# Optimization experiments

Measured on AMD Instinct MI355X. Metric: run time of the kernel, lower is better.

Reference implementation:

```python
import jax, jax.numpy as jnp
import numpy as np

B, HQ, HKV, D = 32, 32, 8, 128
PAGE_SIZE, PAGES_PER_SEQ = 16, 128
NUM_PAGES = B * PAGES_PER_SEQ
MAX_LEN = PAGE_SIZE * PAGES_PER_SEQ  # 2048
SCALING = 0.08838834764831845  # 1/sqrt(128)
LOGIT_CAP = 50.0


def setup_inputs() -> dict:
    key = jax.random.key(0)
    ks = jax.random.split(key, 6)
    q = jax.random.normal(ks[0], (B, HQ * D), jnp.float32)
    k = jax.random.normal(ks[1], (B, HKV * D), jnp.float32)
    v = jax.random.normal(ks[2], (B, HKV * D), jnp.float32)
    k_cache = jax.random.normal(ks[3], (NUM_PAGES, PAGE_SIZE, HKV, D), jnp.float32)
    v_cache = jax.random.normal(ks[4], (NUM_PAGES, PAGE_SIZE, HKV, D), jnp.float32)
    # disjoint page assignment: request b owns pages [b*128, (b+1)*128)
    page_table = jnp.arange(NUM_PAGES, dtype=jnp.int32).reshape(B, PAGES_PER_SEQ)
    seq_lens = jax.random.randint(ks[5], (B,), 1, MAX_LEN + 1, dtype=jnp.int32)
    return dict(q=q, k=k, v=v, k_cache=k_cache, v_cache=v_cache,
                page_table=page_table, seq_lens=seq_lens)


def reference(q, k, v, k_cache, v_cache, page_table, seq_lens):
    # mirror RadixAttention.forward's k.view(-1, Hkv, D) / v.view(-1, Hkv, D)
    kn = k.reshape(B, HKV, D)
    vn = v.reshape(B, HKV, D)

    # save_kv_cache=True: scatter new token (at position seq_len-1) into paged cache
    pos = seq_lens - 1
    page = page_table[jnp.arange(B), pos // PAGE_SIZE]  # [B]
    slot = pos % PAGE_SIZE                              # [B]
    k_cache = k_cache.at[page, slot].set(kn)
    v_cache = v_cache.at[page, slot].set(vn)

    # gather paged KV per request: [B, Lmax, Hkv, D]
    Kb = k_cache[page_table].reshape(B, MAX_LEN, HKV, D)
    Vb = v_cache[page_table].reshape(B, MAX_LEN, HKV, D)

    # GQA: query head h maps to kv head h // (HQ//HKV)
    G = HQ // HKV
    qh = q.reshape(B, HKV, G, D)
    scores = jnp.einsum('bkgd,blkd->bkgl', qh, Kb) * SCALING  # [B,Hkv,G,L]
    scores = LOGIT_CAP * jnp.tanh(scores / LOGIT_CAP)          # logit capping

    valid = jnp.arange(MAX_LEN, dtype=jnp.int32)[None, :] < seq_lens[:, None]  # [B,L]
    scores = jnp.where(valid[:, None, None, :], scores, -jnp.inf)
    p = jax.nn.softmax(scores, axis=-1)
    out = jnp.einsum('bkgl,blkd->bkgd', p, Vb)  # [B,Hkv,G,D]
    return out.reshape(B, HQ * D)
```

## Files before the change

### kernel.cpp

```cpp
#include <hip/hip_runtime.h>
#include <hip/hip_bf16.h>
#include <math.h>

#define BB 32
#define HQ 32
#define HKV 8
#define DD 128
#define PAGE_SZ 16
#define PAGES_PER_SEQ 128
#define MAX_LEN 2048
#define GG 4
#define NCHUNK 8
#define CHUNK 256
#define SCALING 0.08838834764831845f
#define CAP 50.0f
#define WS_STRIDE 520

__device__ __forceinline__ float dpp8_sum(float x) {
    int t;
    t = __builtin_amdgcn_update_dpp(0, __float_as_int(x), 0x111, 0xF, 0xF, true);
    x += __int_as_float(t);
    t = __builtin_amdgcn_update_dpp(0, __float_as_int(x), 0x112, 0xF, 0xF, true);
    x += __int_as_float(t);
    t = __builtin_amdgcn_update_dpp(0, __float_as_int(x), 0x114, 0xF, 0xF, true);
    x += __int_as_float(t);
    return x;
}

__global__ __launch_bounds__(256, 4) void attn_partial(
    const float* __restrict__ q,
    const float* __restrict__ knew,
    const float* __restrict__ vnew,
    const float* __restrict__ k_cache,
    const float* __restrict__ v_cache,
    const int* __restrict__ page_table,
    const int* __restrict__ seq_lens,
    float* __restrict__ ws)
{
    const int idx = blockIdx.x;
    const int c  = idx % NCHUNK;
    const int bh = idx / NCHUNK;
    const int h  = bh % HKV;
    const int b  = bh / HKV;

    const int L  = seq_lens[b];
    const int t0 = c * CHUNK;
    const int t1 = min(t0 + CHUNK, L);
    float* wsb = ws + (size_t)idx * WS_STRIDE;

    if (t0 >= t1) {
        if (threadIdx.x < GG) { wsb[threadIdx.x] = -INFINITY; wsb[GG + threadIdx.x] = 0.0f; }
        return;
    }
    const int NT = t1 - t0;

    __shared__ float s_q[GG][DD];
    __shared__ float s_sc[GG][CHUNK];
    __shared__ float s_red[8][GG * DD];
    __shared__ int   s_pages[CHUNK / PAGE_SZ];
    __shared__ float s_m[GG], s_l[GG];

    const int tid = threadIdx.x;

    for (int i = tid; i < GG * DD; i += 256) {
        int g = i / DD, d = i % DD;
        s_q[g][d] = q[(size_t)b * (HQ * DD) + (h * GG + g) * DD + d];
    }
    if (tid < CHUNK / PAGE_SZ)
        s_pages[tid] = page_table[b * PAGES_PER_SEQ + t0 / PAGE_SZ + tid];
    __syncthreads();

    const float* knew_row = &knew[(size_t)b * (HKV * DD) + h * DD];
    const float* vnew_row = &vnew[(size_t)b * (HKV * DD) + h * DD];

    {
        const int wv = tid >> 6;
        const int ln = tid & 63;
        const int tg = ln >> 3;
        const int lg = ln & 7;

        float4 qf[GG][4];
        #pragma unroll
        for (int g = 0; g < GG; g++)
            #pragma unroll
            for (int p = 0; p < 4; p++)
                qf[g][p] = *(const float4*)&s_q[g][p * 32 + lg * 4];

        const int niter = (NT + 31) >> 5;

#define LOAD_K(I, KV, WT) do {                                                \
        int t_ = t0 + (I) * 32 + wv * 8 + tg;                                 \
        bool vld_ = t_ < t1;                                                  \
        int tc_ = vld_ ? t_ : (t1 - 1);                                       \
        const float* row_;                                                    \
        if (tc_ == L - 1) row_ = knew_row;                                    \
        else {                                                                \
            int page_ = s_pages[(tc_ - t0) >> 4];                             \
            int slot_ = tc_ & (PAGE_SZ - 1);                                  \
            row_ = &k_cache[((size_t)page_ * PAGE_SZ + slot_) * (HKV * DD) + h * DD]; \
        }                                                                     \
        const float4* r4_ = (const float4*)row_;                              \
        KV[0] = r4_[lg]; KV[1] = r4_[8 + lg];                                 \
        KV[2] = r4_[16 + lg]; KV[3] = r4_[24 + lg];                           \
        WT = vld_ ? (t_ - t0) : -1;                                           \
    } while (0)

        float4 kva[4];
        int wta;
        LOAD_K(0, kva, wta);

        for (int i = 0; i < niter; i++) {
            float4 kvb[4];
            int wtb = -1;
            if (i + 1 < niter) LOAD_K(i + 1, kvb, wtb);

            float dots[GG];
            #pragma unroll
            for (int g = 0; g < GG; g++) {
                float s = 0.0f;
                #pragma unroll
                for (int p = 0; p < 4; p++)
                    s += kva[p].x * qf[g][p].x + kva[p].y * qf[g][p].y
                       + kva[p].z * qf[g][p].z + kva[p].w * qf[g][p].w;
                dots[g] = dpp8_sum(s);
            }
            if (lg == 7 && wta >= 0) {
                #pragma unroll
                for (int g = 0; g < GG; g++) s_sc[g][wta] = dots[g];
            }
            #pragma unroll
            for (int p = 0; p < 4; p++) kva[p] = kvb[p];
            wta = wtb;
        }
#undef LOAD_K
    }
    __syncthreads();

    {
        int g  = tid >> 6;
        int wl = tid & 63;
        float mx = -INFINITY;
        for (int t = wl; t < NT; t += 64) {
            float s = s_sc[g][t];
            s = CAP * tanhf(s * (SCALING * (1.0f / CAP)));
            s_sc[g][t] = s;
            mx = fmaxf(mx, s);
        }
        #pragma unroll
        for (int m = 1; m < 64; m <<= 1) mx = fmaxf(mx, __shfl_xor(mx, m));
        float sum = 0.0f;
        for (int t = wl; t < NT; t += 64) {
            float e = __expf(s_sc[g][t] - mx);
            s_sc[g][t] = e;
            sum += e;
        }
        #pragma unroll
        for (int m = 1; m < 64; m <<= 1) sum += __shfl_xor(sum, m);
        if (wl == 0) { s_m[g] = mx; s_l[g] = sum; }
    }
    __syncthreads();

    const int hw = tid >> 5;
    const int ln = tid & 31;

    float4 acc[GG];
    #pragma unroll
    for (int g = 0; g < GG; g++) acc[g] = make_float4(0.f, 0.f, 0.f, 0.f);

    for (int i = 0; i < CHUNK / 32; i++) {
        const int tbase = t0 + i * 32 + hw;
        if (t0 + i * 32 >= t1) break;

        float4 vv[4];
        int   trel[4];
        bool  vld[4];
        #pragma unroll
        for (int j = 0; j < 4; j++) {
            int t = tbase + j * 8;
            vld[j] = (t < t1);
            int tc = vld[j] ? t : tbase;
            trel[j] = tc - t0;
            const float4* vrow;
            if (tc == L - 1) {
                vrow = (const float4*)vnew_row;
            } else {
                int page = s_pages[trel[j] >> 4];
                int slot = tc & (PAGE_SZ - 1);
                vrow = (const float4*)&v_cache[((size_t)page * PAGE_SZ + slot) * (HKV * DD) + h * DD];
            }
            vv[j] = vrow[ln];
        }
        float p[4][GG];
        #pragma unroll
        for (int j = 0; j < 4; j++)
            #pragma unroll
            for (int g = 0; g < GG; g++)
                p[j][g] = vld[j] ? s_sc[g][trel[j]] : 0.0f;

        #pragma unroll
        for (int j = 0; j < 4; j++) {
            #pragma unroll
            for (int g = 0; g < GG; g++) {
                acc[g].x += p[j][g] * vv[j].x; acc[g].y += p[j][g] * vv[j].y;
                acc[g].z += p[j][g] * vv[j].z; acc[g].w += p[j][g] * vv[j].w;
            }
        }
    }
    #pragma unroll
    for (int g = 0; g < GG; g++)
        *(float4*)&s_red[hw][g * DD + 4 * ln] = acc[g];
    __syncthreads();

    for (int i = tid; i < GG * DD; i += 256) {
        float s = 0.f;
        #pragma unroll
        for (int w = 0; w < 8; w++) s += s_red[w][i];
        wsb[8 + i] = s;
    }
    if (tid < GG) { wsb[tid] = s_m[tid]; wsb[GG + tid] = s_l[tid]; }
}

__global__ __launch_bounds__(512) void attn_combine(
    const float* __restrict__ ws, float* __restrict__ out)
{
    const int bh = blockIdx.x;
    const int h  = bh % HKV;
    const int b  = bh / HKV;
    const int tid = threadIdx.x;
    const int g = tid / DD;
    const int d = tid % DD;

    float mv[NCHUNK], lv[NCHUNK];
    float M = -INFINITY;
    #pragma unroll
    for (int c = 0; c < NCHUNK; c++) {
        const float* wsb = ws + (size_t)(bh * NCHUNK + c) * WS_STRIDE;
        mv[c] = wsb[g];
        lv[c] = wsb[GG + g];
        if (lv[c] > 0.0f) M = fmaxf(M, mv[c]);
    }
    float lsum = 0.0f, osum = 0.0f;
    #pragma unroll
    for (int c = 0; c < NCHUNK; c++) {
        if (lv[c] > 0.0f) {
            const float* wsb = ws + (size_t)(bh * NCHUNK + c) * WS_STRIDE;
            float a = __expf(mv[c] - M);
            lsum += lv[c] * a;
            osum += wsb[8 + g * DD + d] * a;
        }
    }
    out[(size_t)b * (HQ * DD) + (h * GG + g) * DD + d] = osum / lsum;
}

extern "C" void kernel_launch(void* const* d_in, const int* in_sizes, int n_in,
                              void* d_out, int out_size, void* d_ws, size_t ws_size,
                              hipStream_t stream) {
    const float* q       = (const float*)d_in[0];
    const float* k       = (const float*)d_in[1];
    const float* v       = (const float*)d_in[2];
    const float* k_cache = (const float*)d_in[3];
    const float* v_cache = (const float*)d_in[4];
    const int* page_table = (const int*)d_in[5];
    const int* seq_lens   = (const int*)d_in[6];
    float* out = (float*)d_out;
    float* ws  = (float*)d_ws;

    attn_partial<<<BB * HKV * NCHUNK, 256, 0, stream>>>(
        q, k, v, k_cache, v_cache, page_table, seq_lens, ws);
    attn_combine<<<BB * HKV, 512, 0, stream>>>(ws, out);
}
```

Before: 475.8 us.

## Process all KV heads per block so each token slab is read contiguously

Each block now covers one batch entry and a 64-token chunk across all 8 KV heads, in place of one head and a 256-token chunk. Each token's full 4 KB K/V slab is then read contiguously by one wave, giving better coalescing than the earlier 512-byte strided row per head. The shared-memory cross-wave reduction is removed because each half-wave owns one head's output directly, and the V loop is software-pipelined four tokens deep. The cost is 32 chunks per sequence, which makes the workspace and the combine pass larger, and per-block work becomes smaller.

```diff
diff --git a/kernel.cpp b/kernel.cpp
--- a/kernel.cpp
+++ b/kernel.cpp
@@ -1,20 +1,19 @@
 #include <hip/hip_runtime.h>
-#include <hip/hip_bf16.h>
 #include <math.h>
 
 #define BB 32
 #define HQ 32
 #define HKV 8
 #define DD 128
+#define GG 4
 #define PAGE_SZ 16
 #define PAGES_PER_SEQ 128
 #define MAX_LEN 2048
-#define GG 4
-#define NCHUNK 8
-#define CHUNK 256
+#define CHUNK 64
+#define NCHUNK 32
 #define SCALING 0.08838834764831845f
 #define CAP 50.0f
-#define WS_STRIDE 520
+#define WS_STRIDE 4160
 
 __device__ __forceinline__ float dpp8_sum(float x) {
     int t;
@@ -38,80 +37,72 @@
     float* __restrict__ ws)
 {
     const int idx = blockIdx.x;
-    const int c  = idx % NCHUNK;
-    const int bh = idx / NCHUNK;
-    const int h  = bh % HKV;
-    const int b  = bh / HKV;
+    const int c = idx % NCHUNK;
+    const int b = idx / NCHUNK;
+    const int tid = threadIdx.x;
 
     const int L  = seq_lens[b];
     const int t0 = c * CHUNK;
+    float* wsb = ws + (size_t)idx * WS_STRIDE;
+
+    if (t0 >= L) {
+        if (tid < 32) { wsb[tid] = -INFINITY; wsb[32 + tid] = 0.0f; }
+        return;
+    }
     const int t1 = min(t0 + CHUNK, L);
-    float* wsb = ws + (size_t)idx * WS_STRIDE;
-
-    if (t0 >= t1) {
-        if (threadIdx.x < GG) { wsb[threadIdx.x] = -INFINITY; wsb[GG + threadIdx.x] = 0.0f; }
-        return;
-    }
     const int NT = t1 - t0;
 
-    __shared__ float s_q[GG][DD];
-    __shared__ float s_sc[GG][CHUNK];
-    __shared__ float s_red[8][GG * DD];
+    __shared__ float s_sc[HKV * GG][CHUNK + 1];
     __shared__ int   s_pages[CHUNK / PAGE_SZ];
-    __shared__ float s_m[GG], s_l[GG];
-
-    const int tid = threadIdx.x;
-
-    for (int i = tid; i < GG * DD; i += 256) {
-        int g = i / DD, d = i % DD;
-        s_q[g][d] = q[(size_t)b * (HQ * DD) + (h * GG + g) * DD + d];
-    }
+    __shared__ float s_m[32], s_l[32];
+
     if (tid < CHUNK / PAGE_SZ)
-        s_pages[tid] = page_table[b * PAGES_PER_SEQ + t0 / PAGE_SZ + tid];
+        s_pages[tid] = page_table[b * PAGES_PER_SEQ + (t0 >> 4) + tid];
     __syncthreads();
 
-    const float* knew_row = &knew[(size_t)b * (HKV * DD) + h * DD];
-    const float* vnew_row = &vnew[(size_t)b * (HKV * DD) + h * DD];
+    const float* knew_b = knew + (size_t)b * (HKV * DD);
+    const float* vnew_b = vnew + (size_t)b * (HKV * DD);
 
     {
         const int wv = tid >> 6;
         const int ln = tid & 63;
-        const int tg = ln >> 3;
+        const int hh = ln >> 3;
         const int lg = ln & 7;
 
         float4 qf[GG][4];
+        const float* qb = q + (size_t)b * (HQ * DD) + (hh * GG) * DD + lg * 4;
         #pragma unroll
         for (int g = 0; g < GG; g++)
             #pragma unroll
             for (int p = 0; p < 4; p++)
-                qf[g][p] = *(const float4*)&s_q[g][p * 32 + lg * 4];
-
-        const int niter = (NT + 31) >> 5;
+                qf[g][p] = *(const float4*)(qb + g * DD + p * 32);
+
+        const int niter = (NT + 3) >> 2;
 
 #define LOAD_K(I, KV, WT) do {                                                \
-        int t_ = t0 + (I) * 32 + wv * 8 + tg;                                 \
-        bool vld_ = t_ < t1;                                                  \
-        int tc_ = vld_ ? t_ : (t1 - 1);                                       \
-        const float* row_;                                                    \
-        if (tc_ == L - 1) row_ = knew_row;                                    \
+        int tt_ = (I) * 4 + wv;                                               \
+        bool vld_ = tt_ < NT;                                                 \
+        int tc_ = vld_ ? tt_ : NT - 1;                                        \
+        int t_ = t0 + tc_;                                                    \
+        const float* slab_;                                                   \
+        if (t_ == L - 1) slab_ = knew_b;             \
         else {                                                                \
-            int page_ = s_pages[(tc_ - t0) >> 4];                             \
-            int slot_ = tc_ & (PAGE_SZ - 1);                                  \
-            row_ = &k_cache[((size_t)page_ * PAGE_SZ + slot_) * (HKV * DD) + h * DD]; \
+            int pg_ = s_pages[tc_ >> 4];                                      \
+            slab_ = k_cache + ((size_t)pg_ * PAGE_SZ + (t_ & (PAGE_SZ - 1)))  \
+                              * (HKV * DD);                                   \
         }                                                                     \
-        const float4* r4_ = (const float4*)row_;                              \
-        KV[0] = r4_[lg]; KV[1] = r4_[8 + lg];                                 \
-        KV[2] = r4_[16 + lg]; KV[3] = r4_[24 + lg];                           \
-        WT = vld_ ? (t_ - t0) : -1;                                           \
+        const float* row_ = slab_ + hh * DD + lg * 4;                         \
+        KV[0] = *(const float4*)(row_);                                       \
+        KV[1] = *(const float4*)(row_ + 32);                                  \
+        KV[2] = *(const float4*)(row_ + 64);                                  \
+        KV[3] = *(const float4*)(row_ + 96);                                  \
+        WT = vld_ ? tt_ : -1;                                                 \
     } while (0)
 
-        float4 kva[4];
-        int wta;
+        float4 kva[4]; int wta;
         LOAD_K(0, kva, wta);
-
         for (int i = 0; i < niter; i++) {
-            float4 kvb[4];
-            int wtb = -1;
+            float4 kvb[4]; int wtb = -1;
             if (i + 1 < niter) LOAD_K(i + 1, kvb, wtb);
 
             float dots[GG];
@@ -126,7 +117,7 @@
             }
             if (lg == 7 && wta >= 0) {
                 #pragma unroll
-                for (int g = 0; g < GG; g++) s_sc[g][wta] = dots[g];
+                for (int g = 0; g < GG; g++) s_sc[hh * GG + g][wta] = dots[g];
             }
             #pragma unroll
             for (int p = 0; p < 4; p++) kva[p] = kvb[p];
@@ -137,87 +128,100 @@
     __syncthreads();
 
     {
-        int g  = tid >> 6;
-        int wl = tid & 63;
+        const int r  = tid >> 3;
+        const int lg = tid & 7;
+        float* row = s_sc[r];
+        const int tb = lg * 8;
         float mx = -INFINITY;
-        for (int t = wl; t < NT; t += 64) {
-            float s = s_sc[g][t];
-            s = CAP * tanhf(s * (SCALING * (1.0f / CAP)));
-            s_sc[g][t] = s;
-            mx = fmaxf(mx, s);
-        }
-        #pragma unroll
-        for (int m = 1; m < 64; m <<= 1) mx = fmaxf(mx, __shfl_xor(mx, m));
+        #pragma unroll
+        for (int j = 0; j < 8; j++) {
+            int t = tb + j;
+            if (t < NT) {
+                float s = row[t];
+                s = CAP * tanhf(s * (SCALING * (1.0f / CAP)));
+                row[t] = s;
+                mx = fmaxf(mx, s);
+            }
+        }
+        mx = fmaxf(mx, __shfl_xor(mx, 1, 8));
+        mx = fmaxf(mx, __shfl_xor(mx, 2, 8));
+        mx = fmaxf(mx, __shfl_xor(mx, 4, 8));
         float sum = 0.0f;
-        for (int t = wl; t < NT; t += 64) {
-            float e = __expf(s_sc[g][t] - mx);
-            s_sc[g][t] = e;
-            sum += e;
-        }
-        #pragma unroll
-        for (int m = 1; m < 64; m <<= 1) sum += __shfl_xor(sum, m);
-        if (wl == 0) { s_m[g] = mx; s_l[g] = sum; }
+        #pragma unroll
+        for (int j = 0; j < 8; j++) {
+            int t = tb + j;
+            if (t < NT) {
+                float e = __expf(row[t] - mx);
+                row[t] = e;
+                sum += e;
+            }
+        }
+        sum += __shfl_xor(sum, 1, 8);
+        sum += __shfl_xor(sum, 2, 8);
+        sum += __shfl_xor(sum, 4, 8);
+        if (lg == 0) { s_m[r] = mx; s_l[r] = sum; }
     }
     __syncthreads();
 
-    const int hw = tid >> 5;
-    const int ln = tid & 31;
-
-    float4 acc[GG];
-    #pragma unroll
-    for (int g = 0; g < GG; g++) acc[g] = make_float4(0.f, 0.f, 0.f, 0.f);
-
-    for (int i = 0; i < CHUNK / 32; i++) {
-        const int tbase = t0 + i * 32 + hw;
-        if (t0 + i * 32 >= t1) break;
-
-        float4 vv[4];
-        int   trel[4];
-        bool  vld[4];
-        #pragma unroll
-        for (int j = 0; j < 4; j++) {
-            int t = tbase + j * 8;
-            vld[j] = (t < t1);
-            int tc = vld[j] ? t : tbase;
-            trel[j] = tc - t0;
-            const float4* vrow;
-            if (tc == L - 1) {
-                vrow = (const float4*)vnew_row;
-            } else {
-                int page = s_pages[trel[j] >> 4];
-                int slot = tc & (PAGE_SZ - 1);
-                vrow = (const float4*)&v_cache[((size_t)page * PAGE_SZ + slot) * (HKV * DD) + h * DD];
-            }
-            vv[j] = vrow[ln];
-        }
-        float p[4][GG];
-        #pragma unroll
-        for (int j = 0; j < 4; j++)
-            #pragma unroll
-            for (int g = 0; g < GG; g++)
-                p[j][g] = vld[j] ? s_sc[g][trel[j]] : 0.0f;
-
-        #pragma unroll
-        for (int j = 0; j < 4; j++) {
-            #pragma unroll
-            for (int g = 0; g < GG; g++) {
-                acc[g].x += p[j][g] * vv[j].x; acc[g].y += p[j][g] * vv[j].y;
-                acc[g].z += p[j][g] * vv[j].z; acc[g].w += p[j][g] * vv[j].w;
-            }
-        }
-    }
-    #pragma unroll
-    for (int g = 0; g < GG; g++)
-        *(float4*)&s_red[hw][g * DD + 4 * ln] = acc[g];
-    __syncthreads();
-
-    for (int i = tid; i < GG * DD; i += 256) {
-        float s = 0.f;
-        #pragma unroll
-        for (int w = 0; w < 8; w++) s += s_red[w][i];
-        wsb[8 + i] = s;
-    }
-    if (tid < GG) { wsb[tid] = s_m[tid]; wsb[GG + tid] = s_l[tid]; }
+    {
+        const int hw = tid >> 5;
+        const int l2 = tid & 31;
+
+        float4 acc[GG];
+        #pragma unroll
+        for (int g = 0; g < GG; g++) acc[g] = make_float4(0.f, 0.f, 0.f, 0.f);
+
+#define LOAD_V(TT, DST) do {                                                  \
+        int tc_ = (TT) < NT ? (TT) : NT - 1;         \
+        int t_ = t0 + tc_;                                                    \
+        const float* slab_;                                                   \
+        if (t_ == L - 1) slab_ = vnew_b;                                      \
+        else {                                                                \
+            int pg_ = s_pages[tc_ >> 4];                                      \
+            slab_ = v_cache + ((size_t)pg_ * PAGE_SZ + (t_ & (PAGE_SZ - 1)))  \
+                              * (HKV * DD);                                   \
+        }                                                                     \
+        DST = *(const float4*)(slab_ + hw * DD + l2 * 4);                     \
+    } while (0)
+
+#define USE_V(TT, VV) do {                                                    \
+        int tt_ = (TT);                                                       \
+        if (tt_ < NT) {                                                       \
+            float p0 = s_sc[hw * GG + 0][tt_];                                \
+            float p1 = s_sc[hw * GG + 1][tt_];                                \
+            float p2 = s_sc[hw * GG + 2][tt_];                                \
+            float p3 = s_sc[hw * GG + 3][tt_];                                \
+            acc[0].x += p0 * VV.x; acc[0].y += p0 * VV.y;                     \
+            acc[0].z += p0 * VV.z; acc[0].w += p0 * VV.w;                     \
+            acc[1].x += p1 * VV.x; acc[1].y += p1 * VV.y;                     \
+            acc[1].z += p1 * VV.z; acc[1].w += p1 * VV.w;                     \
+            acc[2].x += p2 * VV.x; acc[2].y += p2 * VV.y;                     \
+            acc[2].z += p2 * VV.z; acc[2].w += p2 * VV.w;                     \
+            acc[3].x += p3 * VV.x; acc[3].y += p3 * VV.y;                     \
+            acc[3].z += p3 * VV.z; acc[3].w += p3 * VV.w;                     \
+        }                                                                     \
+    } while (0)
+
+        float4 v0, v1, v2, v3;
+        LOAD_V(0, v0); LOAD_V(1, v1); LOAD_V(2, v2); LOAD_V(3, v3);
+        for (int base = 0; base < NT; base += 4) {
+            float4 n0, n1, n2, n3;
+            LOAD_V(base + 4, n0); LOAD_V(base + 5, n1);
+            LOAD_V(base + 6, n2); LOAD_V(base + 7, n3);
+            USE_V(base + 0, v0);
+            USE_V(base + 1, v1);
+            USE_V(base + 2, v2);
+            USE_V(base + 3, v3);
+            v0 = n0; v1 = n1; v2 = n2; v3 = n3;
+        }
+#undef USE_V
+#undef LOAD_V
+
+        #pragma unroll
+        for (int g = 0; g < GG; g++)
+            *(float4*)&wsb[64 + (hw * GG + g) * DD + l2 * 4] = acc[g];
+        if (tid < 32) { wsb[tid] = s_m[tid]; wsb[32 + tid] = s_l[tid]; }
+    }
 }
 
 __global__ __launch_bounds__(512) void attn_combine(
@@ -227,29 +231,30 @@
     const int h  = bh % HKV;
     const int b  = bh / HKV;
     const int tid = threadIdx.x;
-    const int g = tid / DD;
-    const int d = tid % DD;
+    const int g = tid >> 7;
+    const int d = tid & 127;
+    const int r = h * GG + g;
 
     float mv[NCHUNK], lv[NCHUNK];
     float M = -INFINITY;
     #pragma unroll
-    for (int c = 0; c < NCHUNK; c++) {
-        const float* wsb = ws + (size_t)(bh * NCHUNK + c) * WS_STRIDE;
-        mv[c] = wsb[g];
-        lv[c] = wsb[GG + g];
-        if (lv[c] > 0.0f) M = fmaxf(M, mv[c]);
+    for (int cc = 0; cc < NCHUNK; cc++) {
+        const float* wsb = ws + (size_t)(b * NCHUNK + cc) * WS_STRIDE;
+        mv[cc] = wsb[r];
+        lv[cc] = wsb[32 + r];
+        if (lv[cc] > 0.0f) M = fmaxf(M, mv[cc]);
     }
     float lsum = 0.0f, osum = 0.0f;
     #pragma unroll
-    for (int c = 0; c < NCHUNK; c++) {
-        if (lv[c] > 0.0f) {
-            const float* wsb = ws + (size_t)(bh * NCHUNK + c) * WS_STRIDE;
-            float a = __expf(mv[c] - M);
-            lsum += lv[c] * a;
-            osum += wsb[8 + g * DD + d] * a;
-        }
-    }
-    out[(size_t)b * (HQ * DD) + (h * GG + g) * DD + d] = osum / lsum;
+    for (int cc = 0; cc < NCHUNK; cc++) {
+        if (lv[cc] > 0.0f) {
+            const float* wsb = ws + (size_t)(b * NCHUNK + cc) * WS_STRIDE;
+            float a = __expf(mv[cc] - M);
+            lsum += lv[cc] * a;
+            osum += wsb[64 + r * DD + d] * a;
+        }
+    }
+    out[(size_t)b * (HQ * DD) + r * DD + d] = osum / lsum;
 }
 
 extern "C" void kernel_launch(void* const* d_in, const int* in_sizes, int n_in,
@@ -265,7 +270,7 @@
     float* out = (float*)d_out;
     float* ws  = (float*)d_ws;
 
-    attn_partial<<<BB * HKV * NCHUNK, 256, 0, stream>>>(
+    attn_partial<<<BB * NCHUNK, 256, 0, stream>>>(
         q, k, v, k_cache, v_cache, page_table, seq_lens, ws);
     attn_combine<<<BB * HKV, 512, 0, stream>>>(ws, out);
 }
```

Result: slower. 486.5 us (+2.2%).
